# Optimization experiments

Measured on AMD Instinct MI355X. Metric: run time of the kernel, lower is better.

Reference implementation:

```python
import jax, jax.numpy as jnp
import numpy as np

HEADS = 8
DIM_HEAD = 32
EPS = 1e-5


def _rel_index(h, w):
    # matches Attention._generate_relative_index (static, computed on host)
    coords = np.stack(np.meshgrid(np.arange(h), np.arange(w), indexing='ij')).reshape(2, -1)
    rel = coords[:, :, None] - coords[:, None, :]  # [2, n, n]
    rel[0] += h - 1
    rel[1] += w - 1
    rel[0] *= 2 * w - 1
    idx = rel.sum(0).reshape(-1)
    # torch.clamp(relative_index, 0, max_index) -- indices are already in range here
    return jnp.asarray(np.clip(idx, 0, (2 * h - 1) * (2 * w - 1) - 1))


def _layernorm(x, g, b):
    m = jnp.mean(x, axis=-1, keepdims=True)
    v = jnp.var(x, axis=-1, keepdims=True)
    return (x - m) * jax.lax.rsqrt(v + EPS) * g + b


def setup_inputs() -> dict:
    key = jax.random.key(0)
    ks = jax.random.split(key, 6)
    B, C, H, W = 64, 384, 16, 16
    inner = HEADS * DIM_HEAD  # 256
    hid = 4 * C               # 1536
    def nrm(k, shape, s=0.02):
        return jax.random.normal(k, shape, jnp.float32) * s
    return {
        'x': jax.random.normal(ks[0], (B, C, H, W), jnp.float32),
        'ln1_g': jnp.ones((C,), jnp.float32),
        'ln1_b': jnp.zeros((C,), jnp.float32),
        'w_qkv': nrm(ks[1], (C, 3 * inner)),
        'bias_table': nrm(ks[2], ((2 * H - 1) * (2 * W - 1), HEADS)),
        'w_out': nrm(ks[3], (inner, C)),
        'b_out': jnp.zeros((C,), jnp.float32),
        'ln2_g': jnp.ones((C,), jnp.float32),
        'ln2_b': jnp.zeros((C,), jnp.float32),
        'w_ff1': nrm(ks[4], (C, hid)),
        'b_ff1': jnp.zeros((hid,), jnp.float32),
        'w_ff2': nrm(ks[5], (hid, C)),
        'b_ff2': jnp.zeros((C,), jnp.float32),
    }


def reference(x, ln1_g, ln1_b, w_qkv, bias_table, w_out, b_out,
              ln2_g, ln2_b, w_ff1, b_ff1, w_ff2, b_ff2):
    B, C, H, W = x.shape
    n = H * W
    t = x.reshape(B, C, n).transpose(0, 2, 1)  # [B, n, C]

    # --- attention branch (PreNorm(LayerNorm) -> Attention) ---
    a = _layernorm(t, ln1_g, ln1_b)
    qkv = a @ w_qkv  # [B, n, 3*inner]
    q, k, v = jnp.split(qkv, 3, axis=-1)
    def split_heads(z):
        return z.reshape(B, n, HEADS, DIM_HEAD).transpose(0, 2, 1, 3)  # [B, h, n, d]
    q, k, v = split_heads(q), split_heads(k), split_heads(v)
    dots = jnp.einsum('bhid,bhjd->bhij', q, k) * (DIM_HEAD ** -0.5)
    idx = _rel_index(H, W)  # [n*n]
    rel_bias = bias_table[idx].reshape(n, n, HEADS).transpose(2, 0, 1)[None]  # [1, h, n, n]
    attn = jax.nn.softmax(dots + rel_bias, axis=-1)
    o = jnp.einsum('bhij,bhjd->bhid', attn, v)
    o = o.transpose(0, 2, 1, 3).reshape(B, n, HEADS * DIM_HEAD)
    attn_out = o @ w_out + b_out  # to_out Linear (dropout=0)

    # --- feedforward branch (PreNorm(LayerNorm) -> FFN) ---
    f = _layernorm(t, ln2_g, ln2_b)
    f = jax.nn.gelu(f @ w_ff1 + b_ff1, approximate=False) @ w_ff2 + b_ff2

    y = t + attn_out + f  # x_adjusted + attn_out + ff_out
    return y.transpose(0, 2, 1).reshape(B, C, H, W)
```

## Files before the change

### kernel.cpp

```cpp
#include <hip/hip_runtime.h>

typedef __bf16 bf16;
typedef __bf16 bf16x8 __attribute__((ext_vector_type(8)));
typedef float f32x4 __attribute__((ext_vector_type(4)));

__device__ __forceinline__ void gll16(const void* g, void* l) {
    __builtin_amdgcn_global_load_lds((const __attribute__((address_space(1))) void*)g,
                                     (__attribute__((address_space(3))) void*)l, 16, 0, 0);
}

#define WBAR(N) asm volatile("s_waitcnt vmcnt(" #N ")\n\ts_barrier" ::: "memory")

__device__ __forceinline__ float gelu_f(float v) {
    float x2 = v * v;
    float sn = v * fmaf(-0.0713540072f, x2, -1.5957691216f);
    float e  = __expf(sn);
    return v * __builtin_amdgcn_rcpf(1.0f + e);
}

__launch_bounds__(256)
__global__ void prep_kernel(const float* __restrict__ wqkv, const float* __restrict__ wout,
                            const float* __restrict__ wff1, const float* __restrict__ wff2,
                            bf16* __restrict__ wqkvT, bf16* __restrict__ woutT,
                            bf16* __restrict__ wff1T, bf16* __restrict__ wff2T,
                            const float* __restrict__ x,
                            const float* __restrict__ g1, const float* __restrict__ b1,
                            const float* __restrict__ g2, const float* __restrict__ b2,
                            bf16* __restrict__ a, bf16* __restrict__ f) {
    __shared__ __align__(16) float smem[12672 + 512 + 64];
    const int tid = threadIdx.x;
    int g = blockIdx.x;
    if (g < 1536) {
        float (*tl)[33] = (float (*)[33])smem;
        const float* in; bf16* out; int R, Cc, bx, by;
        if (g < 288)       { in = wqkv; out = wqkvT; R = 384;  Cc = 768;  bx = g % 24; by = g / 24; }
        else if (g < 384)  { g -= 288; in = wout; out = woutT; R = 256;  Cc = 384;  bx = g % 12; by = g / 12; }
        else if (g < 960)  { g -= 384; in = wff1; out = wff1T; R = 384;  Cc = 1536; bx = g % 48; by = g / 48; }
        else               { g -= 960; in = wff2; out = wff2T; R = 1536; Cc = 384;  bx = g % 12; by = g / 12; }
        const int c0 = bx * 32, r0 = by * 32;
        const int cl = tid & 31, r8 = tid >> 5;
#pragma unroll
        for (int k = 0; k < 4; k++) {
            int r = k * 8 + r8;
            tl[r][cl] = in[(size_t)(r0 + r) * Cc + c0 + cl];
        }
        __syncthreads();
#pragma unroll
        for (int k = 0; k < 4; k++) {
            int cc = k * 8 + r8;
            out[(size_t)(c0 + cc) * R + r0 + cl] = (bf16)tl[cl][cc];
        }
        return;
    }
    g -= 1536;
    float (*tile)[33] = (float (*)[33])smem;
    float (*S)[32]  = (float (*)[32])(smem + 12672);
    float (*SS)[32] = (float (*)[32])(smem + 12928);
    float* Mn = smem + 13184;
    float* Rs = smem + 13216;
    const int bb = g >> 3;
    const int i0 = (g & 7) * 32;
    {
        const int i_l = tid & 31, c_l = tid >> 5;
        const size_t base = (size_t)bb * 384 * 256 + i0 + i_l;
#pragma unroll 6
        for (int c = c_l; c < 384; c += 8)
            tile[c][i_l] = x[base + (size_t)c * 256];
    }
    __syncthreads();
    {
        const int i_s = tid & 31, p = tid >> 5;
        float s = 0.f, ss = 0.f;
#pragma unroll 6
        for (int j = 0; j < 48; j++) {
            float v = tile[p * 48 + j][i_s];
            s += v; ss += v * v;
        }
        S[p][i_s] = s; SS[p][i_s] = ss;
    }
    __syncthreads();
    if (tid < 32) {
        float t1 = 0.f, t2 = 0.f;
#pragma unroll
        for (int p = 0; p < 8; p++) { t1 += S[p][tid]; t2 += SS[p][tid]; }
        float mean = t1 * (1.0f / 384.0f);
        float var  = t2 * (1.0f / 384.0f) - mean * mean;
        Mn[tid] = mean;
        Rs[tid] = rsqrtf(var + 1e-5f);
    }
    __syncthreads();
    const int lane = tid & 63, w = tid >> 6;
#pragma unroll
    for (int rr = 0; rr < 8; rr++) {
        const int i = w * 8 + rr;
        const float mean = Mn[i], rstd = Rs[i];
        const size_t orow = ((size_t)bb * 256 + i0 + i) * 384;
#pragma unroll
        for (int pass = 0; pass < 6; pass++) {
            const int c = pass * 64 + lane;
            float nh = (tile[c][i] - mean) * rstd;
            a[orow + c] = (bf16)(nh * g1[c] + b1[c]);
            f[orow + c] = (bf16)(nh * g2[c] + b2[c]);
        }
    }
}

#define STAGE128(buf, kb)                                                   \
    {                                                                       \
        bf16* sA = lds + (buf) * 8192;                                      \
        bf16* sB = sA + 4096;                                               \
        gll16(Abase + (size_t)r0 * K + (kb) + ksw, sA + c0 * 8);            \
        gll16(Abase + (size_t)r1 * K + (kb) + ksw, sA + c1 * 8);            \
        gll16(Bbase + (size_t)r0 * K + (kb) + ksw, sB + c0 * 8);            \
        gll16(Bbase + (size_t)r1 * K + (kb) + ksw, sB + c1 * 8);            \
    }
#define COMPUTE128(buf)                                                     \
    {                                                                       \
        const bf16* sA = lds + (buf) * 8192;                                \
        const bf16* sB = sA + 4096;                                         \
        bf16x8 af[4], bfr[4];                                               \
        _Pragma("unroll") for (int i = 0; i < 4; i++)                       \
            af[i] = *(const bf16x8*)(sA + (wm + i * 16 + l16) * 32 + rsw);  \
        _Pragma("unroll") for (int j = 0; j < 4; j++)                       \
            bfr[j] = *(const bf16x8*)(sB + (wn + j * 16 + l16) * 32 + rsw); \
        _Pragma("unroll") for (int i = 0; i < 4; i++)                       \
            _Pragma("unroll") for (int j = 0; j < 4; j++)                   \
                acc[i][j] = __builtin_amdgcn_mfma_f32_16x16x32_bf16(af[i], bfr[j], acc[i][j], 0, 0, 0); \
    }
#define GEMM128_PRO_KLOOP                                                            \
    const int tid = threadIdx.x;                                                     \
    const int g = blockIdx.x;                                                        \
    const int x_ = (g >> 3) % nx;                                                    \
    const int y_ = (g & 7) + 8 * (g / (8 * nx));                                     \
    const int m0 = y_ * 128, n0 = x_ * 128;                                          \
    const int lane = tid & 63, w = tid >> 6;                                         \
    const int l16 = lane & 15, quad = lane >> 4;                                     \
    const int wm = (w & 1) * 64, wn = (w >> 1) * 64;                                 \
    f32x4 zero = {0.f, 0.f, 0.f, 0.f};                                               \
    f32x4 acc[4][4];                                                                 \
    _Pragma("unroll") for (int i = 0; i < 4; i++)                                    \
        _Pragma("unroll") for (int j = 0; j < 4; j++) acc[i][j] = zero;              \
    const int c0 = tid, c1 = tid + 256;                                              \
    const int r0 = c0 >> 2, r1 = c1 >> 2;                                            \
    const int ksw = (((tid & 3) ^ ((tid >> 3) & 3)) * 8);   \
    const int rsw = ((quad ^ ((l16 >> 1) & 3)) * 8);              \
    const bf16* Abase = A + (size_t)m0 * K;                                          \
    const bf16* Bbase = Bt + (size_t)n0 * K;                                         \
    STAGE128(0, 0);                                                                  \
    STAGE128(1, 32);                                                                 \
    const int nt = K >> 5;                                                           \
    int t = 0;                                                                       \
    for (; t < nt - 2; ++t) {                                                        \
        WBAR(4);                                                                     \
        STAGE128((t + 2) % 3, (t + 2) * 32);                                         \
        COMPUTE128(t % 3);                                                           \
    }                                                                                \
    WBAR(4); COMPUTE128(t % 3); ++t;                                                 \
    WBAR(0); COMPUTE128(t % 3);                                                      \
    __syncthreads();

template <int EPI>
__launch_bounds__(256)
__global__ void gemm_bt(const bf16* __restrict__ A, const bf16* __restrict__ Bt,
                        const float* __restrict__ bias, bf16* __restrict__ C,
                        int M, int N, int K, int nx) {
    __shared__ __align__(16) bf16 lds[24576];
    GEMM128_PRO_KLOOP
#pragma unroll
    for (int j = 0; j < 4; j++) {
        const int col = wn + j * 16 + l16;
        float bv = 0.f;
        if (EPI >= 1) bv = bias[n0 + col];
#pragma unroll
        for (int i = 0; i < 4; i++) {
            const int row0 = wm + i * 16 + quad * 4;
#pragma unroll
            for (int r = 0; r < 4; r++) {
                float v = acc[i][j][r] + bv;
                if (EPI == 2) v = gelu_f(v);
                lds[(row0 + r) * 128 + col] = (bf16)v;
            }
        }
    }
    __syncthreads();
#pragma unroll
    for (int it = 0; it < 8; it++) {
        const int ch = tid + it * 256;
        const int row = ch >> 4, cc = (ch & 15) * 8;
        *(bf16x8*)(C + (size_t)(m0 + row) * N + n0 + cc) = *(const bf16x8*)(lds + row * 128 + cc);
    }
}

__launch_bounds__(256)
__global__ void gemm_bt_tr128(const bf16* __restrict__ A, const bf16* __restrict__ Bt,
                              const float* __restrict__ bias, bf16* __restrict__ Ct,
                              int M, int N, int K, int nx) {
    __shared__ __align__(16) bf16 lds[24576];
    GEMM128_PRO_KLOOP
#pragma unroll
    for (int j = 0; j < 4; j++) {
        const int col = wn + j * 16 + l16;
        const float bv = bias[n0 + col];
#pragma unroll
        for (int i = 0; i < 4; i++) {
            const int row0 = wm + i * 16 + quad * 4;
#pragma unroll
            for (int r = 0; r < 4; r++)
                lds[col * 132 + row0 + r] = (bf16)(acc[i][j][r] + bv);
        }
    }
    __syncthreads();
    const int b = m0 >> 8, ib = m0 & 255;
#pragma unroll
    for (int it = 0; it < 8; it++) {
        const int ch = tid + it * 256;
        const int cl = ch >> 4, ic = (ch & 15) * 8;
        *(bf16x8*)(Ct + ((size_t)(b * 384 + n0 + cl) * 256 + ib + ic)) =
            *(const bf16x8*)(lds + cl * 132 + ic);
    }
}

__launch_bounds__(256)
__global__ void gemm_bt_fin128(const bf16* __restrict__ A, const bf16* __restrict__ Bt,
                               const float* __restrict__ bias,
                               const float* __restrict__ xres, const bf16* __restrict__ attn_t,
                               float* __restrict__ out, int M, int N, int K, int nx) {
    __shared__ __align__(16) bf16 lds[24576];
    GEMM128_PRO_KLOOP
#pragma unroll
    for (int j = 0; j < 4; j++) {
        const int col = wn + j * 16 + l16;
        const float bv = bias[n0 + col];
#pragma unroll
        for (int i = 0; i < 4; i++) {
            const int row0 = wm + i * 16 + quad * 4;
#pragma unroll
            for (int r = 0; r < 4; r++)
                lds[col * 132 + row0 + r] = (bf16)(acc[i][j][r] + bv);
        }
    }
    __syncthreads();
    const int b = m0 >> 8, ib = m0 & 255;
#pragma unroll
    for (int it = 0; it < 8; it++) {
        const int ch = tid + it * 256;
        const int cl = ch >> 4, ic = (ch & 15) * 8;
        const size_t base = (size_t)(b * 384 + n0 + cl) * 256 + ib + ic;
        bf16x8 ff = *(const bf16x8*)(lds + cl * 132 + ic);
        bf16x8 at = *(const bf16x8*)(attn_t + base);
        const f32x4* xr = (const f32x4*)(xres + base);
        f32x4 o0, o1;
#pragma unroll
        for (int e = 0; e < 4; e++) o0[e] = xr[0][e] + (float)at[e] + (float)ff[e];
#pragma unroll
        for (int e = 0; e < 4; e++) o1[e] = xr[1][e] + (float)at[e + 4] + (float)ff[e + 4];
        ((f32x4*)(out + base))[0] = o0;
        ((f32x4*)(out + base))[1] = o1;
    }
}

__launch_bounds__(256)
__global__ void attn_kernel(const bf16* __restrict__ qkv,
                            const float* __restrict__ btab,
                            bf16* __restrict__ o) {
    __shared__ float sbias[961];
    __shared__ __align__(16) bf16 sK[256 * 32];
    __shared__ __align__(16) bf16 sVt[32][264];
    __shared__ __align__(16) bf16 sP[4][16][264];
    const int tid = threadIdx.x;
    const int g = blockIdx.x;
    const int h  = (g >> 3) & 7;
    const int bb = (g & 7) + 8 * (g >> 6);
    const int lane = tid & 63, w = tid >> 6;
    const int l16 = lane & 15, quad = lane >> 4;
    const int rsw = ((quad ^ ((l16 >> 1) & 3)) * 8);
    const size_t qkvb = (size_t)bb * 256 * 768;
    const bf16* Qbase = qkv + qkvb + h * 32;
    const bf16* Kbase = qkv + qkvb + 256 + h * 32;
    const bf16* Vbase = qkv + qkvb + 512 + h * 32;

    for (int e = tid; e < 961; e += 256) sbias[e] = btab[e * 8 + h];
#pragma unroll
    for (int it = 0; it < 4; it++) {
        const int ch = it * 256 + tid;
        const int row = ch >> 2;
        const int d8 = (((ch & 3) ^ ((ch >> 3) & 3)) * 8);
        gll16(Kbase + (size_t)row * 768 + d8, sK + ch * 8);
    }
#pragma unroll
    for (int it = 0; it < 4; it++) {
        const int ch = it * 256 + tid;
        const int k = ch >> 2, d8 = (ch & 3) * 8;
        bf16x8 vv = *(const bf16x8*)(Vbase + (size_t)k * 768 + d8);
#pragma unroll
        for (int j = 0; j < 8; j++)
            sVt[d8 + j][k] = vv[j];
    }
    __syncthreads();

    f32x4 zero = {0.f, 0.f, 0.f, 0.f};
    for (int qc = 0; qc < 4; qc++) {
        const int qbase = qc * 64 + w * 16;
        bf16x8 qf = *(const bf16x8*)(Qbase + (size_t)(qbase + l16) * 768 + quad * 8);
        f32x4 s[16];
#pragma unroll
        for (int kt = 0; kt < 16; kt++) {
            bf16x8 kf = *(const bf16x8*)(sK + (kt * 16 + l16) * 32 + rsw);
            s[kt] = __builtin_amdgcn_mfma_f32_16x16x32_bf16(qf, kf, zero, 0, 0, 0);
        }
        const int qi0 = qbase + quad * 4;
        float mx[4] = {-1e30f, -1e30f, -1e30f, -1e30f};
#pragma unroll
        for (int kt = 0; kt < 16; kt++) {
            const int j = kt * 16 + l16;
            const int yj = j >> 4, xj = j & 15;
#pragma unroll
            for (int r = 0; r < 4; r++) {
                const int q = qi0 + r;
                const int tix = ((q >> 4) - yj + 15) * 31 + ((q & 15) - xj + 15);
                float v = s[kt][r] * 0.17677669529663687f + sbias[tix];
                s[kt][r] = v;
                mx[r] = fmaxf(mx[r], v);
            }
        }
#pragma unroll
        for (int r = 0; r < 4; r++)
            for (int msk = 1; msk < 16; msk <<= 1)
                mx[r] = fmaxf(mx[r], __shfl_xor(mx[r], msk, 64));
        float sum[4] = {0.f, 0.f, 0.f, 0.f};
#pragma unroll
        for (int kt = 0; kt < 16; kt++)
#pragma unroll
            for (int r = 0; r < 4; r++) {
                float e = __expf(s[kt][r] - mx[r]);
                s[kt][r] = e;
                sum[r] += e;
            }
#pragma unroll
        for (int r = 0; r < 4; r++) {
            for (int msk = 1; msk < 16; msk <<= 1)
                sum[r] += __shfl_xor(sum[r], msk, 64);
            sum[r] = 1.0f / sum[r];
        }
#pragma unroll
        for (int kt = 0; kt < 16; kt++)
#pragma unroll
            for (int r = 0; r < 4; r++)
                sP[w][quad * 4 + r][kt * 16 + l16] = (bf16)(s[kt][r] * sum[r]);
        f32x4 oacc[2];
        oacc[0] = zero; oacc[1] = zero;
#pragma unroll
        for (int ks = 0; ks < 8; ks++) {
            bf16x8 pf = *(const bf16x8*)(&sP[w][l16][ks * 32 + quad * 8]);
#pragma unroll
            for (int dt = 0; dt < 2; dt++) {
                bf16x8 vf = *(const bf16x8*)(&sVt[dt * 16 + l16][ks * 32 + quad * 8]);
                oacc[dt] = __builtin_amdgcn_mfma_f32_16x16x32_bf16(pf, vf, oacc[dt], 0, 0, 0);
            }
        }
#pragma unroll
        for (int dt = 0; dt < 2; dt++)
#pragma unroll
            for (int r = 0; r < 4; r++)
                o[(size_t)(bb * 256 + qbase + quad * 4 + r) * 256 + h * 32 + dt * 16 + l16] = (bf16)oacc[dt][r];
    }
}

extern "C" void kernel_launch(void* const* d_in, const int* in_sizes, int n_in,
                              void* d_out, int out_size, void* d_ws, size_t ws_size,
                              hipStream_t stream) {
    const float* x    = (const float*)d_in[0];
    const float* g1   = (const float*)d_in[1];
    const float* b1   = (const float*)d_in[2];
    const float* wqkv = (const float*)d_in[3];
    const float* btab = (const float*)d_in[4];
    const float* wout = (const float*)d_in[5];
    const float* bout = (const float*)d_in[6];
    const float* g2   = (const float*)d_in[7];
    const float* b2   = (const float*)d_in[8];
    const float* wff1 = (const float*)d_in[9];
    const float* bff1 = (const float*)d_in[10];
    const float* wff2 = (const float*)d_in[11];
    const float* bff2 = (const float*)d_in[12];
    float* out = (float*)d_out;

    bf16* ws = (bf16*)d_ws;
    const size_t NA = 6291456;
    bf16* wqkvT = ws;
    bf16* woutT = wqkvT + 294912;
    bf16* wff1T = woutT + 98304;
    bf16* wff2T = wff1T + 589824;
    bf16* f_buf    = ws + 1572864;
    bf16* attn_t   = f_buf + NA;
    bf16* R        = attn_t + NA;
    bf16* a_buf    = R;
    bf16* qkv_buf  = R + NA;
    bf16* o_buf    = R;
    bf16* ffh_buf  = R;

    dim3 b256(256);
    prep_kernel<<<2048, b256, 0, stream>>>(wqkv, wout, wff1, wff2, wqkvT, woutT, wff1T, wff2T,
                                           x, g1, b1, g2, b2, a_buf, f_buf);

    gemm_bt<0><<<6 * 128, b256, 0, stream>>>(a_buf, wqkvT, nullptr, qkv_buf, 16384, 768, 384, 6);
    attn_kernel<<<512, b256, 0, stream>>>(qkv_buf, btab, o_buf);
    gemm_bt_tr128<<<3 * 128, b256, 0, stream>>>(o_buf, woutT, bout, attn_t, 16384, 384, 256, 3);
    gemm_bt<2><<<12 * 128, b256, 0, stream>>>(f_buf, wff1T, bff1, ffh_buf, 16384, 1536, 384, 12);
    gemm_bt_fin128<<<3 * 128, b256, 0, stream>>>(ffh_buf, wff2T, bff2, x, attn_t, out,
                                                 16384, 384, 1536, 3);
}
```

Baseline: 227.0 us.

## Co-schedule attention with FF1 GEMM and fuse out-proj into FF2 K-loop

Attention and the FF1 GELU GEMM now run as one launch: every fourth block runs attention and the other three run GEMM tiles, sharing one dynamic-role shared-memory buffer. The out-projection is folded into the FF2 GEMM by concatenating the two K ranges (1536 + 256) into a single accumulator loop with a summed bias. This removes two launches and the bf16 attn_t intermediate round-trip through global memory. In exchange, buffers no longer alias so the workspace grows, and the 70 KB shared-memory footprint of the combined kernel may limit occupancy for the GEMM blocks.

```diff
diff --git a/kernel.cpp b/kernel.cpp
--- a/kernel.cpp
+++ b/kernel.cpp
@@ -127,11 +127,9 @@
             _Pragma("unroll") for (int j = 0; j < 4; j++)                   \
                 acc[i][j] = __builtin_amdgcn_mfma_f32_16x16x32_bf16(af[i], bfr[j], acc[i][j], 0, 0, 0); \
     }
-#define GEMM128_PRO_KLOOP                                                            \
-    const int tid = threadIdx.x;                                                     \
-    const int g = blockIdx.x;                                                        \
-    const int x_ = (g >> 3) % nx;                                                    \
-    const int y_ = (g & 7) + 8 * (g / (8 * nx));                                     \
+#define GEMM128_PRO_KLOOP(BID)                                                       \
+    const int x_ = ((BID) >> 3) % nx;                                                \
+    const int y_ = ((BID) & 7) + 8 * ((BID) / (8 * nx));                             \
     const int m0 = y_ * 128, n0 = x_ * 128;                                          \
     const int lane = tid & 63, w = tid >> 6;                                         \
     const int l16 = lane & 15, quad = lane >> 4;                                     \
@@ -142,8 +140,8 @@
         _Pragma("unroll") for (int j = 0; j < 4; j++) acc[i][j] = zero;              \
     const int c0 = tid, c1 = tid + 256;                                              \
     const int r0 = c0 >> 2, r1 = c1 >> 2;                                            \
-    const int ksw = (((tid & 3) ^ ((tid >> 3) & 3)) * 8);   \
-    const int rsw = ((quad ^ ((l16 >> 1) & 3)) * 8);              \
+    const int ksw = (((tid & 3) ^ ((tid >> 3) & 3)) * 8);                            \
+    const int rsw = ((quad ^ ((l16 >> 1) & 3)) * 8);                                 \
     const bf16* Abase = A + (size_t)m0 * K;                                          \
     const bf16* Bbase = Bt + (size_t)n0 * K;                                         \
     STAGE128(0, 0);                                                                  \
@@ -165,7 +163,8 @@
                         const float* __restrict__ bias, bf16* __restrict__ C,
                         int M, int N, int K, int nx) {
     __shared__ __align__(16) bf16 lds[24576];
-    GEMM128_PRO_KLOOP
+    const int tid = threadIdx.x;
+    GEMM128_PRO_KLOOP(blockIdx.x)
 #pragma unroll
     for (int j = 0; j < 4; j++) {
         const int col = wn + j * 16 + l16;
@@ -192,85 +191,48 @@
 }
 
 __launch_bounds__(256)
-__global__ void gemm_bt_tr128(const bf16* __restrict__ A, const bf16* __restrict__ Bt,
-                              const float* __restrict__ bias, bf16* __restrict__ Ct,
-                              int M, int N, int K, int nx) {
-    __shared__ __align__(16) bf16 lds[24576];
-    GEMM128_PRO_KLOOP
-#pragma unroll
-    for (int j = 0; j < 4; j++) {
-        const int col = wn + j * 16 + l16;
-        const float bv = bias[n0 + col];
-#pragma unroll
-        for (int i = 0; i < 4; i++) {
-            const int row0 = wm + i * 16 + quad * 4;
-#pragma unroll
-            for (int r = 0; r < 4; r++)
-                lds[col * 132 + row0 + r] = (bf16)(acc[i][j][r] + bv);
-        }
-    }
-    __syncthreads();
-    const int b = m0 >> 8, ib = m0 & 255;
-#pragma unroll
-    for (int it = 0; it < 8; it++) {
-        const int ch = tid + it * 256;
-        const int cl = ch >> 4, ic = (ch & 15) * 8;
-        *(bf16x8*)(Ct + ((size_t)(b * 384 + n0 + cl) * 256 + ib + ic)) =
-            *(const bf16x8*)(lds + cl * 132 + ic);
-    }
-}
-
-__launch_bounds__(256)
-__global__ void gemm_bt_fin128(const bf16* __restrict__ A, const bf16* __restrict__ Bt,
-                               const float* __restrict__ bias,
-                               const float* __restrict__ xres, const bf16* __restrict__ attn_t,
-                               float* __restrict__ out, int M, int N, int K, int nx) {
-    __shared__ __align__(16) bf16 lds[24576];
-    GEMM128_PRO_KLOOP
-#pragma unroll
-    for (int j = 0; j < 4; j++) {
-        const int col = wn + j * 16 + l16;
-        const float bv = bias[n0 + col];
-#pragma unroll
-        for (int i = 0; i < 4; i++) {
-            const int row0 = wm + i * 16 + quad * 4;
-#pragma unroll
-            for (int r = 0; r < 4; r++)
-                lds[col * 132 + row0 + r] = (bf16)(acc[i][j][r] + bv);
-        }
-    }
-    __syncthreads();
-    const int b = m0 >> 8, ib = m0 & 255;
-#pragma unroll
-    for (int it = 0; it < 8; it++) {
-        const int ch = tid + it * 256;
-        const int cl = ch >> 4, ic = (ch & 15) * 8;
-        const size_t base = (size_t)(b * 384 + n0 + cl) * 256 + ib + ic;
-        bf16x8 ff = *(const bf16x8*)(lds + cl * 132 + ic);
-        bf16x8 at = *(const bf16x8*)(attn_t + base);
-        const f32x4* xr = (const f32x4*)(xres + base);
-        f32x4 o0, o1;
-#pragma unroll
-        for (int e = 0; e < 4; e++) o0[e] = xr[0][e] + (float)at[e] + (float)ff[e];
-#pragma unroll
-        for (int e = 0; e < 4; e++) o1[e] = xr[1][e] + (float)at[e + 4] + (float)ff[e + 4];
-        ((f32x4*)(out + base))[0] = o0;
-        ((f32x4*)(out + base))[1] = o1;
-    }
-}
-
-__launch_bounds__(256)
-__global__ void attn_kernel(const bf16* __restrict__ qkv,
-                            const float* __restrict__ btab,
-                            bf16* __restrict__ o) {
-    __shared__ float sbias[961];
-    __shared__ __align__(16) bf16 sK[256 * 32];
-    __shared__ __align__(16) bf16 sVt[32][264];
-    __shared__ __align__(16) bf16 sP[4][16][264];
+__global__ void stage3_kernel(const bf16* __restrict__ A, const bf16* __restrict__ Bt,
+                              const float* __restrict__ bias, bf16* __restrict__ C,
+                              const bf16* __restrict__ qkv, const float* __restrict__ btab,
+                              bf16* __restrict__ o) {
+    __shared__ __align__(16) char smem[70928];
     const int tid = threadIdx.x;
-    const int g = blockIdx.x;
-    const int h  = (g >> 3) & 7;
-    const int bb = (g & 7) + 8 * (g >> 6);
+    const int gg = blockIdx.x;
+    if (gg & 3) {
+        const int bid = (gg >> 2) * 3 + (gg & 3) - 1;
+        bf16* lds = (bf16*)smem;
+        const int K = 384, N = 1536, nx = 12;
+        GEMM128_PRO_KLOOP(bid)
+#pragma unroll
+        for (int j = 0; j < 4; j++) {
+            const int col = wn + j * 16 + l16;
+            const float bv = bias[n0 + col];
+#pragma unroll
+            for (int i = 0; i < 4; i++) {
+                const int row0 = wm + i * 16 + quad * 4;
+#pragma unroll
+                for (int r = 0; r < 4; r++) {
+                    float v = gelu_f(acc[i][j][r] + bv);
+                    lds[(row0 + r) * 128 + col] = (bf16)v;
+                }
+            }
+        }
+        __syncthreads();
+#pragma unroll
+        for (int it = 0; it < 8; it++) {
+            const int ch = tid + it * 256;
+            const int row = ch >> 4, cc = (ch & 15) * 8;
+            *(bf16x8*)(C + (size_t)(m0 + row) * N + n0 + cc) = *(const bf16x8*)(lds + row * 128 + cc);
+        }
+        return;
+    }
+    const int aid = gg >> 2;
+    float* sbias = (float*)smem;
+    bf16* sK = (bf16*)(smem + 3856);
+    bf16 (*sVt)[264] = (bf16 (*)[264])(smem + 20240);
+    bf16 (*sP)[16][264] = (bf16 (*)[16][264])(smem + 37136);
+    const int h  = (aid >> 3) & 7;
+    const int bb = (aid & 7) + 8 * (aid >> 6);
     const int lane = tid & 63, w = tid >> 6;
     const int l16 = lane & 15, quad = lane >> 4;
     const int rsw = ((quad ^ ((l16 >> 1) & 3)) * 8);
@@ -363,6 +325,95 @@
 #pragma unroll
             for (int r = 0; r < 4; r++)
                 o[(size_t)(bb * 256 + qbase + quad * 4 + r) * 256 + h * 32 + dt * 16 + l16] = (bf16)oacc[dt][r];
+    }
+}
+
+__launch_bounds__(256)
+__global__ void fin_dual(const bf16* __restrict__ Af, const bf16* __restrict__ Bf,
+                         const bf16* __restrict__ Ao, const bf16* __restrict__ Bo,
+                         const float* __restrict__ bff2, const float* __restrict__ bout,
+                         const float* __restrict__ xres, float* __restrict__ out, int nx) {
+    __shared__ __align__(16) bf16 lds[24576];
+    const int tid = threadIdx.x;
+    const int g = blockIdx.x;
+    const int x_ = (g >> 3) % nx;
+    const int y_ = (g & 7) + 8 * (g / (8 * nx));
+    const int m0 = y_ * 128, n0 = x_ * 128;
+    const int lane = tid & 63, w = tid >> 6;
+    const int l16 = lane & 15, quad = lane >> 4;
+    const int wm = (w & 1) * 64, wn = (w >> 1) * 64;
+    f32x4 acc[4][4];
+    { f32x4 z = {0.f, 0.f, 0.f, 0.f};
+#pragma unroll
+      for (int i = 0; i < 4; i++)
+#pragma unroll
+          for (int j = 0; j < 4; j++) acc[i][j] = z; }
+    const int c0 = tid, c1 = tid + 256;
+    const int r0 = c0 >> 2, r1 = c1 >> 2;
+    const int ksw = (((tid & 3) ^ ((tid >> 3) & 3)) * 8);
+    const int rsw = ((quad ^ ((l16 >> 1) & 3)) * 8);
+    const bf16* A1 = Af + (size_t)m0 * 1536;
+    const bf16* B1 = Bf + (size_t)n0 * 1536;
+    const bf16* A2 = Ao + (size_t)m0 * 256;
+    const bf16* B2 = Bo + (size_t)n0 * 256;
+
+#define STGD(buf, s)                                                                \
+    {   bf16* sA = lds + (buf) * 8192;                                              \
+        bf16* sB = sA + 4096;                                                       \
+        if ((s) < 48) {                                                             \
+            const int kb = (s) * 32;                                                \
+            gll16(A1 + (size_t)r0 * 1536 + kb + ksw, sA + c0 * 8);                  \
+            gll16(A1 + (size_t)r1 * 1536 + kb + ksw, sA + c1 * 8);                  \
+            gll16(B1 + (size_t)r0 * 1536 + kb + ksw, sB + c0 * 8);                  \
+            gll16(B1 + (size_t)r1 * 1536 + kb + ksw, sB + c1 * 8);                  \
+        } else {                                                                    \
+            const int kb = ((s) - 48) * 32;                                         \
+            gll16(A2 + (size_t)r0 * 256 + kb + ksw, sA + c0 * 8);                   \
+            gll16(A2 + (size_t)r1 * 256 + kb + ksw, sA + c1 * 8);                   \
+            gll16(B2 + (size_t)r0 * 256 + kb + ksw, sB + c0 * 8);                   \
+            gll16(B2 + (size_t)r1 * 256 + kb + ksw, sB + c1 * 8);                   \
+        } }
+
+    STGD(0, 0); STGD(1, 1);
+    int s = 0;
+    for (; s < 54; ++s) {
+        WBAR(4);
+        STGD((s + 2) % 3, s + 2);
+        COMPUTE128(s % 3);
+    }
+    WBAR(4); COMPUTE128(s % 3); ++s;
+    WBAR(0); COMPUTE128(s % 3);
+    __syncthreads();
+#undef STGD
+
+#pragma unroll
+    for (int j = 0; j < 4; j++) {
+        const int col = wn + j * 16 + l16;
+        const float bv = bff2[n0 + col] + bout[n0 + col];
+#pragma unroll
+        for (int i = 0; i < 4; i++) {
+            const int row0 = wm + i * 16 + quad * 4;
+#pragma unroll
+            for (int r = 0; r < 4; r++)
+                lds[col * 132 + row0 + r] = (bf16)(acc[i][j][r] + bv);
+        }
+    }
+    __syncthreads();
+    const int b = m0 >> 8, ib = m0 & 255;
+#pragma unroll
+    for (int it = 0; it < 8; it++) {
+        const int ch = tid + it * 256;
+        const int cl = ch >> 4, ic = (ch & 15) * 8;
+        const size_t base = (size_t)(b * 384 + n0 + cl) * 256 + ib + ic;
+        bf16x8 ff = *(const bf16x8*)(lds + cl * 132 + ic);
+        const f32x4* xr = (const f32x4*)(xres + base);
+        f32x4 o0, o1;
+#pragma unroll
+        for (int e = 0; e < 4; e++) o0[e] = xr[0][e] + (float)ff[e];
+#pragma unroll
+        for (int e = 0; e < 4; e++) o1[e] = xr[1][e] + (float)ff[e + 4];
+        ((f32x4*)(out + base))[0] = o0;
+        ((f32x4*)(out + base))[1] = o1;
     }
 }
 
@@ -386,26 +437,20 @@
 
     bf16* ws = (bf16*)d_ws;
     const size_t NA = 6291456;
-    bf16* wqkvT = ws;
-    bf16* woutT = wqkvT + 294912;
-    bf16* wff1T = woutT + 98304;
-    bf16* wff2T = wff1T + 589824;
-    bf16* f_buf    = ws + 1572864;
-    bf16* attn_t   = f_buf + NA;
-    bf16* R        = attn_t + NA;
-    bf16* a_buf    = R;
-    bf16* qkv_buf  = R + NA;
-    bf16* o_buf    = R;
-    bf16* ffh_buf  = R;
+    bf16* wqkvT   = ws;
+    bf16* woutT   = wqkvT + 294912;
+    bf16* wff1T   = woutT + 98304;
+    bf16* wff2T   = wff1T + 589824;
+    bf16* f_buf   = ws + 1572864;
+    bf16* a_buf   = f_buf + NA;
+    bf16* qkv_buf = a_buf + NA;
+    bf16* o_buf   = qkv_buf + 12582912;
+    bf16* ffh_buf = o_buf + 4194304;
 
     dim3 b256(256);
     prep_kernel<<<2048, b256, 0, stream>>>(wqkv, wout, wff1, wff2, wqkvT, woutT, wff1T, wff2T,
                                            x, g1, b1, g2, b2, a_buf, f_buf);
-
     gemm_bt<0><<<6 * 128, b256, 0, stream>>>(a_buf, wqkvT, nullptr, qkv_buf, 16384, 768, 384, 6);
-    attn_kernel<<<512, b256, 0, stream>>>(qkv_buf, btab, o_buf);
-    gemm_bt_tr128<<<3 * 128, b256, 0, stream>>>(o_buf, woutT, bout, attn_t, 16384, 384, 256, 3);
-    gemm_bt<2><<<12 * 128, b256, 0, stream>>>(f_buf, wff1T, bff1, ffh_buf, 16384, 1536, 384, 12);
-    gemm_bt_fin128<<<3 * 128, b256, 0, stream>>>(ffh_buf, wff2T, bff2, x, attn_t, out,
-                                                 16384, 384, 1536, 3);
-}
+    stage3_kernel<<<2048, b256, 0, stream>>>(f_buf, wff1T, bff1, ffh_buf, qkv_buf, btab, o_buf);
+    fin_dual<<<3 * 128, b256, 0, stream>>>(ffh_buf, wff2T, o_buf, woutT, bff2, bout, x, out, 3);
+}
```

After: 235.4 us. +3.7%, slower.
